# Optimization experiments

Hardware: AMD Instinct MI355X
Metric: run time of the kernel (lower is better)

The kernel has to match this reference:

```python
import jax, jax.numpy as jnp
import numpy as np

B, NG, DEG, CW, OUT = 8, 16384, 16, 64, 256  # graphs, nodes/graph, avg degree, conv_width, output_dim


def _sage(x, src, dst, mask, Wl, bl, Wr):
    # PyG SAGEConv: mean-aggregate neighbors (src -> dst), lin_l(agg)+bias + lin_r(x)
    N = x.shape[0]
    s = jax.ops.segment_sum(x[src] * mask[:, None], dst, num_segments=N)
    c = jax.ops.segment_sum(mask, dst, num_segments=N)
    mean = s / jnp.maximum(c, 1.0)[:, None]
    return mean @ Wl.T + bl + x @ Wr.T


def _gcn(x, src, dst, mask, W, b):
    # PyG GCNConv: self-loops + symmetric deg^{-1/2} normalization; edge_weight == mask
    N = x.shape[0]
    xw = x @ W.T
    deg = 1.0 + jax.ops.segment_sum(mask, dst, num_segments=N)
    dis = jax.lax.rsqrt(deg)
    norm = dis[src] * mask * dis[dst]
    out = jax.ops.segment_sum(xw[src] * norm[:, None], dst, num_segments=N)
    return out + xw * (dis * dis)[:, None] + b


def _topk(x, src, dst, mask, w, n):
    # PyG TopKPooling: score = tanh(x.w/||w||), keep top ceil(0.5*n) per graph,
    # gate kept features by score, re-index edges (here: fixed-size edges + mask)
    score = jnp.tanh((x @ w) / jnp.linalg.norm(w))
    k = (n + 1) // 2
    vals, idx = jax.lax.top_k(score.reshape(B, n), k)  # [B,k], descending like PyG
    perm = (idx + (jnp.arange(B) * n)[:, None]).reshape(-1)  # global old indices
    x_new = x[perm] * vals.reshape(-1)[:, None]
    newpos = jnp.full((B * n,), -1, jnp.int32).at[perm].set(
        jnp.arange(B * k, dtype=jnp.int32))
    ns, nd = newpos[src], newpos[dst]
    m = mask * ((ns >= 0) & (nd >= 0)).astype(x.dtype)
    return x_new, jnp.maximum(ns, 0), jnp.maximum(nd, 0), m, k


def _readout(x, k):
    # [global_max_pool, global_mean_pool] per graph
    xr = x.reshape(B, k, -1)
    return jnp.concatenate([xr.max(axis=1), xr.mean(axis=1)], axis=1)


def setup_inputs() -> dict:
    key = jax.random.key(0)
    ks = jax.random.split(key, 24)
    N, Eg = B * NG, NG * DEG
    off = (jnp.arange(B) * NG)[:, None]
    src = (jax.random.randint(ks[0], (B, Eg), 0, NG) + off).reshape(-1)
    dst = (jax.random.randint(ks[1], (B, Eg), 0, NG) + off).reshape(-1)
    edge_index = jnp.stack([src, dst]).astype(jnp.int32)
    x = jax.random.normal(ks[2], (N, 2), jnp.float32)

    def xav(k, o, i):
        return jax.random.normal(k, (o, i), jnp.float32) * np.float32(np.sqrt(2.0 / (o + i)))

    def vec(k, d):
        return jax.random.normal(k, (d,), jnp.float32) * np.float32(1.0 / np.sqrt(d))

    return dict(
        x=x, edge_index=edge_index,
        Wl1=xav(ks[3], CW, 2), bl1=vec(ks[4], CW), Wr1=xav(ks[5], CW, 2),
        Wl2=xav(ks[6], CW, CW), bl2=vec(ks[7], CW), Wr2=xav(ks[8], CW, CW),
        W4=xav(ks[9], CW, CW), b4=vec(ks[10], CW),
        W5=xav(ks[11], CW, CW), b5=vec(ks[12], CW),
        wp1=vec(ks[13], CW), wp2=vec(ks[14], CW), wp4=vec(ks[15], CW), wp5=vec(ks[16], CW),
        Wa=xav(ks[17], 128, 2 * CW), ba=vec(ks[18], 128),
        Wb=xav(ks[19], 64, 128), bb=vec(ks[20], 64),
        Wc=xav(ks[21], OUT, 64), bc=vec(ks[22], OUT),
    )


def reference(x, edge_index, Wl1, bl1, Wr1, Wl2, bl2, Wr2, W4, b4, W5, b5,
              wp1, wp2, wp4, wp5, Wa, ba, Wb, bb, Wc, bc):
    src, dst = edge_index[0], edge_index[1]
    mask = jnp.ones(src.shape[0], x.dtype)
    n = NG
    h = jax.nn.relu(_sage(x, src, dst, mask, Wl1, bl1, Wr1))
    h, src, dst, mask, n = _topk(h, src, dst, mask, wp1, n)
    x1 = _readout(h, n)
    h = jax.nn.relu(_sage(h, src, dst, mask, Wl2, bl2, Wr2))
    h, src, dst, mask, n = _topk(h, src, dst, mask, wp2, n)
    x2 = _readout(h, n)
    h = jax.nn.relu(_gcn(h, src, dst, mask, W4, b4))
    h, src, dst, mask, n = _topk(h, src, dst, mask, wp4, n)
    x4 = _readout(h, n)
    h = jax.nn.relu(_gcn(h, src, dst, mask, W5, b5))
    h, src, dst, mask, n = _topk(h, src, dst, mask, wp5, n)
    x5 = _readout(h, n)
    z = x1 + x2 + x4 + x5  # [B, 2*CW]
    z = jax.nn.relu(z @ Wa.T + ba)
    z = jax.nn.relu(z @ Wb.T + bb)
    z = z @ Wc.T + bc
    return jax.nn.softmax(z, axis=1)
```

## Files before the change

### kernel.cpp

```cpp
#include <hip/hip_runtime.h>
#include <math.h>

constexpr int Bq  = 8;
constexpr int NGq = 16384;
constexpr int Nq  = Bq * NGq;
constexpr int Eq  = Nq * 16;
constexpr int Eg  = Eq / 8;
constexpr int BCAP = 8192;

constexpr int P1 = 0;
constexpr int P2 = 524288;
constexpr int P3 = 786432;
constexpr int P4 = 917504;
constexpr int PTOT = 983040;

__global__ void k_prep(const float* __restrict__ Wl2, const float* __restrict__ Wr2,
                       const float* __restrict__ W4, const float* __restrict__ W5,
                       const float* __restrict__ Wa, const float* __restrict__ Wb,
                       const float* __restrict__ Wc,
                       const float* __restrict__ w1, const float* __restrict__ w2,
                       const float* __restrict__ w4p, const float* __restrict__ w5p,
                       float* __restrict__ wT, float* __restrict__ wMT,
                       float* __restrict__ winv, int* __restrict__ bcur) {
    int t = threadIdx.x, b = blockIdx.x;
    if (b < 4) {
        const float* in = (b == 0) ? Wl2 : (b == 1) ? Wr2 : (b == 2) ? W4 : W5;
        float* out = wT + (size_t)b * 4096;
        for (int i = t; i < 4096; i += 256) {
            int r = i >> 6, c = i & 63;
            out[c * 64 + r] = in[r * 64 + c];
        }
    } else if (b == 4) {
        float* WaT = wMT;
        for (int i = t; i < 16384; i += 256) {
            int r = i >> 7, c = i & 127;
            WaT[c * 128 + r] = Wa[r * 128 + c];
        }
    } else if (b == 5) {
        float* WbT = wMT + 16384;
        for (int i = t; i < 8192; i += 256) {
            int r = i >> 7, c = i & 127;
            WbT[c * 64 + r] = Wb[r * 128 + c];
        }
    } else if (b == 6) {
        float* WcT = wMT + 16384 + 8192;
        for (int i = t; i < 16384; i += 256) {
            int r = i >> 6, c = i & 63;
            WcT[c * 256 + r] = Wc[r * 64 + c];
        }
    } else {
        int vsel = t >> 6, lane = t & 63;
        const float* wp = (vsel == 0) ? w1 : (vsel == 1) ? w2 : (vsel == 2) ? w4p : w5p;
        float v = wp[lane];
        float ww = v * v;
        for (int o = 32; o; o >>= 1) ww += __shfl_xor(ww, o);
        if (lane == 0) winv[vsel] = 1.0f / sqrtf(ww);
        for (int i = t; i < 512; i += 256) bcur[i] = 0;
    }
}

__global__ void k_csr_a(const int* __restrict__ src, const int* __restrict__ dst,
                        int* __restrict__ bcur, unsigned* __restrict__ pairs) {
    __shared__ int hist[512];
    __shared__ int base[512];
    __shared__ int lcur[512];
    int t = threadIdx.x;
    int blk = blockIdx.x;
    int e0 = blk * 8192;
    int bk[8]; unsigned p[8];
#pragma unroll
    for (int i = 0; i < 8; i++) {
        int e = e0 + i * 1024 + t;
        int d = dst[e];
        bk[i] = d >> 8;
        p[i] = ((unsigned)(d & 255) << 24) | (unsigned)src[e];
    }
    if (t < 512) hist[t] = 0;
    __syncthreads();
#pragma unroll
    for (int i = 0; i < 8; i++) atomicAdd(&hist[bk[i]], 1);
    __syncthreads();
    if (t < 512) {
        int h = hist[t];
        base[t] = h ? atomicAdd(&bcur[t], h) : 0;
        lcur[t] = 0;
    }
    __syncthreads();
#pragma unroll
    for (int i = 0; i < 8; i++) {
        int b = bk[i];
        int r = base[b] + atomicAdd(&lcur[b], 1);
        if (r < BCAP) pairs[(size_t)b * BCAP + r] = p[i];
    }
}

__global__ void k_csr_b(const int* __restrict__ bcnt, const unsigned* __restrict__ pairs,
                        const float2* __restrict__ x2,
                        int* __restrict__ off, int* __restrict__ deg,
                        int* __restrict__ csrc, float2* __restrict__ mean) {
    __shared__ int lcnt[256];
    __shared__ int lcur[256];
    __shared__ int wsum[4];
    int b = blockIdx.x, t = threadIdx.x;
    int beg = b * BCAP;
    int c0 = bcnt[b]; if (c0 > BCAP) c0 = BCAP;
    int end = beg + c0;
    lcnt[t] = 0;
    __syncthreads();
    for (int i = beg + t; i < end; i += 256)
        atomicAdd(&lcnt[pairs[i] >> 24], 1);
    __syncthreads();
    int v = lcnt[t];
    int lane = t & 63, wv = t >> 6;
    int val = v;
    for (int o = 1; o < 64; o <<= 1) {
        int u = __shfl_up(val, o);
        if (lane >= o) val += u;
    }
    if (lane == 63) wsum[wv] = val;
    __syncthreads();
    int add = 0;
    for (int q = 0; q < wv; q++) add += wsum[q];
    int gpos = beg + val + add - v;
    off[b * 256 + t] = gpos;
    deg[b * 256 + t] = v;
    lcur[t] = gpos;
    __syncthreads();
    for (int i = beg + t; i < end; i += 256) {
        unsigned p = pairs[i];
        int pos = atomicAdd(&lcur[p >> 24], 1);
        csrc[pos] = (int)(p & 0x00FFFFFFu);
    }
    __syncthreads();
    float s0 = 0.f, s1 = 0.f;
    for (int e = gpos; e < gpos + v; e++) {
        float2 xv = x2[csrc[e]];
        s0 += xv.x; s1 += xv.y;
    }
    float c = fmaxf((float)v, 1.0f);
    mean[b * 256 + t] = make_float2(s0 / c, s1 / c);
}

__global__ void k_sage1e(const float* __restrict__ x, const float2* __restrict__ mean,
                         const float* __restrict__ Wl, const float* __restrict__ bl,
                         const float* __restrict__ Wr, const float* __restrict__ wp,
                         const float* __restrict__ invn,
                         float* __restrict__ out, float* __restrict__ score) {
    int blk = blockIdx.x;
    int g = blk & 7, i = blk >> 3;
    int wv = threadIdx.x >> 6, j = threadIdx.x & 63;
    int n = g * NGq + i * 4 + wv;
    float2 xn = ((const float2*)x)[n];
    float2 m = mean[n];
    float2 wl = ((const float2*)Wl)[j];
    float2 wr = ((const float2*)Wr)[j];
    float v = wl.x * m.x + wl.y * m.y + bl[j] + wr.x * xn.x + wr.y * xn.y;
    v = fmaxf(v, 0.f);
    out[n * 64 + j] = v;
    float d = v * wp[j];
    for (int o = 32; o; o >>= 1) d += __shfl_xor(d, o);
    if (j == 0) score[n] = d * invn[0];
}

__device__ __forceinline__
void lin_rows(const float* __restrict__ h, const float* __restrict__ WT,
              const float* __restrict__ bias, float* __restrict__ o,
              int Nn, int nblk, int blk0) {
    int j = threadIdx.x & 63, wv = threadIdx.x >> 6;
    float wreg[64];
#pragma unroll
    for (int q = 0; q < 64; q++) wreg[q] = WT[q * 64 + j];
    float bj = bias ? bias[j] : 0.f;
    int stride = nblk * 4;
    for (int n = blk0 * 4 + wv; n < Nn; n += stride) {
        float iv = h[(size_t)n * 64 + j];
        float a0 = 0.f, a1 = 0.f, a2 = 0.f, a3 = 0.f;
#pragma unroll
        for (int q = 0; q < 16; q++) {
            float s0 = __int_as_float(__builtin_amdgcn_readlane(__float_as_int(iv), q));
            float s1 = __int_as_float(__builtin_amdgcn_readlane(__float_as_int(iv), q + 16));
            float s2 = __int_as_float(__builtin_amdgcn_readlane(__float_as_int(iv), q + 32));
            float s3 = __int_as_float(__builtin_amdgcn_readlane(__float_as_int(iv), q + 48));
            a0 += s0 * wreg[q];
            a1 += s1 * wreg[q + 16];
            a2 += s2 * wreg[q + 32];
            a3 += s3 * wreg[q + 48];
        }
        o[(size_t)n * 64 + j] = (a0 + a1) + (a2 + a3) + bj;
    }
}

__global__ __launch_bounds__(256, 4)
void k_linf(const float* __restrict__ h,
            const float* __restrict__ WT1, float* __restrict__ o1, int linB1,
            const float* __restrict__ WT2, const float* __restrict__ bias,
            float* __restrict__ o2, int linB2,
            int Nn,
            const int* __restrict__ off, const int* __restrict__ deg,
            const int* __restrict__ csrc,
            const int* __restrict__ map, const int* __restrict__ orig,
            float* __restrict__ dis, int ng) {
    int blk = blockIdx.x;
    if (blk < linB1) {
        lin_rows(h, WT1, nullptr, o1, Nn, linB1, blk);
    } else if (blk < linB1 + linB2) {
        lin_rows(h, WT2, bias, o2, Nn, linB2, blk - linB1);
    } else {
        int b2 = blk - linB1 - linB2;
        int g = b2 & 7, i = b2 >> 3;
        int wv = threadIdx.x >> 6, j = threadIdx.x & 63;
        int n = g * ng + i * 4 + wv;
        int o = orig[n];
        int beg = off[o], end = beg + deg[o];
        int c = 0;
        for (int base = beg; base < end; base += 64) {
            int d = end - base; if (d > 64) d = 64;
            int cs = (j < d) ? map[csrc[base + j]] : -1;
            c += __popcll(__ballot(cs >= 0));
        }
        if (j == 0) dis[n] = 1.0f / sqrtf(1.0f + (float)c);
    }
}

template<int M>
__global__ void k_topk(float* __restrict__ score, int* __restrict__ newpos,
                       int* __restrict__ perm, int* __restrict__ map, int mode,
                       const int* __restrict__ orig_in, int* __restrict__ orig_out,
                       int og) {
    constexpr int n = M * 1024;
    constexpr int k = n / 2;
    __shared__ unsigned hist[256];
    __shared__ unsigned sh_pfx, sh_msk, sh_rem;
    __shared__ int sh_eqtot, sh_ctr;
    __shared__ int wtot[16];
    __shared__ int runTie, runGt;
    int t = threadIdx.x, b = blockIdx.x;
    int base = b * n;
    int lane = t & 63, wv = t >> 6;

    unsigned kr[M];
#pragma unroll
    for (int i = 0; i < M; i++) {
        unsigned u = __float_as_uint(score[base + t + (i << 10)]);
        kr[i] = u ^ ((u >> 31) ? 0xFFFFFFFFu : 0x80000000u);
    }
    if (t < 256) hist[t] = 0;
    if (t == 0) { sh_pfx = 0; sh_msk = 0; sh_rem = (unsigned)k;
                  sh_eqtot = 0; sh_ctr = 0; runTie = 0; runGt = 0; }
    __syncthreads();

    for (int shift = 24; shift >= 0; shift -= 8) {
        unsigned pfx = sh_pfx, msk = sh_msk;
#pragma unroll
        for (int i = 0; i < M; i++)
            if ((kr[i] & msk) == pfx) atomicAdd(&hist[(kr[i] >> shift) & 255], 1u);
        __syncthreads();
        if (t < 64) {
            unsigned rem = sh_rem;
            unsigned c0 = hist[255 - (t * 4 + 0)];
            unsigned c1 = hist[255 - (t * 4 + 1)];
            unsigned c2 = hist[255 - (t * 4 + 2)];
            unsigned c3 = hist[255 - (t * 4 + 3)];
            unsigned s = c0 + c1 + c2 + c3;
            unsigned sc = s;
            for (int o = 1; o < 64; o <<= 1) {
                unsigned u = __shfl_up(sc, o);
                if (t >= o) sc += u;
            }
            unsigned run = sc - s;
            unsigned cc[4] = {c0, c1, c2, c3};
#pragma unroll
            for (int q = 0; q < 4; q++) {
                unsigned incl = run + cc[q];
                if (run < rem && incl >= rem) {
                    int bb = 255 - (t * 4 + q);
                    sh_rem = rem - run;
                    sh_pfx = pfx | ((unsigned)bb << shift);
                    sh_msk = msk | (255u << shift);
                }
                run = incl;
            }
        }
        __syncthreads();
        if (t < 256) hist[t] = 0;
        __syncthreads();
    }
    unsigned K = sh_pfx;
    int T = (int)sh_rem;

    int le = 0;
#pragma unroll
    for (int i = 0; i < M; i++) le += (kr[i] == K) ? 1 : 0;
    for (int o = 32; o; o >>= 1) le += __shfl_xor(le, o);
    if (lane == 0) atomicAdd(&sh_eqtot, le);
    __syncthreads();

    if (sh_eqtot == T) {
#pragma unroll
        for (int i = 0; i < M; i++) {
            int cur = base + t + (i << 10);
            bool kept = kr[i] >= K;
            unsigned long long mk = __ballot(kept);
            int pos = 0;
            if (mk) {
                int fl = __ffsll(mk) - 1;
                int bp = 0;
                if (lane == fl) bp = atomicAdd(&sh_ctr, __popcll(mk));
                bp = __shfl(bp, fl);
                pos = bp + __popcll(mk & ((1ull << lane) - 1ull));
            }
            if (kept && pos < k) {
                newpos[cur] = b * k + pos;
                perm[b * k + pos] = cur;
                if (og) orig_out[b * k + pos] = (og == 1) ? cur : orig_in[cur];
                unsigned ob = (kr[i] & 0x80000000u) ? (kr[i] ^ 0x80000000u) : ~kr[i];
                score[cur] = tanhf(__uint_as_float(ob));
            } else newpos[cur] = -1;
        }
    } else {
        for (int i = 0; i < M; i++) {
            unsigned key = kr[i];
            int gt = key > K ? 1 : 0;
            int eq = key == K ? 1 : 0;
            int val = (eq << 16) | gt;
            for (int o = 1; o < 64; o <<= 1) {
                int v = __shfl_up(val, o);
                if (lane >= o) val += v;
            }
            if (lane == 63) wtot[wv] = val;
            __syncthreads();
            int add = 0;
            for (int q = 0; q < 16; q++) if (q < wv) add += wtot[q];
            val += add;
            int eqIncl = val >> 16, gtIncl = val & 0xffff;
            int eqExcl = eqIncl - eq, gtExcl = gtIncl - gt;
            int kept = gt | (eq & ((runTie + eqExcl) < T ? 1 : 0));
            int cur = base + t + (i << 10);
            if (kept) {
                int selEqBefore = runTie + eqExcl; if (selEqBefore > T) selEqBefore = T;
                int nl = runGt + gtExcl + selEqBefore;
                if (nl < k) {
                    newpos[cur] = b * k + nl;
                    perm[b * k + nl] = cur;
                    if (og) orig_out[b * k + nl] = (og == 1) ? cur : orig_in[cur];
                    unsigned ob = (key & 0x80000000u) ? (key ^ 0x80000000u) : ~key;
                    score[cur] = tanhf(__uint_as_float(ob));
                } else newpos[cur] = -1;
            } else newpos[cur] = -1;
            __syncthreads();
            if (t == 1023) { runTie += eqIncl; runGt += gtIncl; }
            __syncthreads();
        }
    }

    if (mode) {
        __syncthreads();
        int gbase = b * NGq;
        for (int i2 = t; i2 < NGq; i2 += 1024) {
            int gi = gbase + i2;
            if (mode == 1) map[gi] = newpos[gi];
            else { int m = map[gi]; map[gi] = (m >= 0) ? newpos[m] : -1; }
        }
    }
}

__global__ void k_compact4(const float* __restrict__ hin, const float* __restrict__ score,
                           const int* __restrict__ perm, float* __restrict__ hout, int k,
                           float* __restrict__ partial) {
    __shared__ float sred[2][16][64];
    int blk = blockIdx.x;
    int g = blk & 7, i = blk >> 3;
    int t = threadIdx.x;
    int r = t >> 4, c = t & 15;
    int nn = g * k + i * 16 + r;
    int old = perm[nn];
    float4 v = ((const float4*)(hin + (size_t)old * 64))[c];
    float sc = score[old];
    v.x *= sc; v.y *= sc; v.z *= sc; v.w *= sc;
    ((float4*)(hout + (size_t)nn * 64))[c] = v;
    sred[0][r][c * 4 + 0] = v.x; sred[0][r][c * 4 + 1] = v.y;
    sred[0][r][c * 4 + 2] = v.z; sred[0][r][c * 4 + 3] = v.w;
    sred[1][r][c * 4 + 0] = v.x; sred[1][r][c * 4 + 1] = v.y;
    sred[1][r][c * 4 + 2] = v.z; sred[1][r][c * 4 + 3] = v.w;
    __syncthreads();
    if (t < 64) {
        float mx = sred[0][0][t], sm = sred[1][0][t];
        for (int rr = 1; rr < 16; rr++) {
            mx = fmaxf(mx, sred[0][rr][t]);
            sm += sred[1][rr][t];
        }
        partial[(size_t)blk * 128 + t] = mx;
        partial[(size_t)blk * 128 + 64 + t] = sm;
    }
}

__global__ void k_sage_gather2(const float* __restrict__ gl, const int* __restrict__ off,
                               const int* __restrict__ deg, const int* __restrict__ csrc,
                               const int* __restrict__ map,
                               const int* __restrict__ orig, const float* __restrict__ wp,
                               const float* __restrict__ invn,
                               float* __restrict__ own_in,
                               float* __restrict__ out, float* __restrict__ score, int ng) {
    int blk = blockIdx.x;
    int g = blk & 7, i = blk >> 3;
    int wv = threadIdx.x >> 6, l = threadIdx.x & 63;
    int n = g * ng + i * 4 + wv;
    int o = orig[n];
    int beg = off[o], end = beg + deg[o];
    int fg = l & 15, es = l >> 4;
    float4 own = make_float4(0.f, 0.f, 0.f, 0.f);
    if (es == 0) own = ((const float4*)(own_in + (size_t)n * 64))[fg];
    float4 acc = make_float4(0.f, 0.f, 0.f, 0.f);
    int cnt = 0;
    for (int base = beg; base < end; base += 64) {
        int d = end - base; if (d > 64) d = 64;
        int cs = (l < d) ? map[csrc[base + l]] : -1;
        cnt += __popcll(__ballot(cs >= 0));
        for (int e = 0; e < d; e += 4) {
            int c = __shfl(cs, e + es);
            if (c >= 0) {
                float4 v = ((const float4*)(gl + (size_t)c * 64))[fg];
                acc.x += v.x; acc.y += v.y; acc.z += v.z; acc.w += v.w;
            }
        }
    }
    acc.x += __shfl_xor(acc.x, 16); acc.y += __shfl_xor(acc.y, 16);
    acc.z += __shfl_xor(acc.z, 16); acc.w += __shfl_xor(acc.w, 16);
    acc.x += __shfl_xor(acc.x, 32); acc.y += __shfl_xor(acc.y, 32);
    acc.z += __shfl_xor(acc.z, 32); acc.w += __shfl_xor(acc.w, 32);
    float c = fmaxf((float)cnt, 1.0f);
    float4 v;
    v.x = fmaxf(acc.x / c + own.x, 0.f);
    v.y = fmaxf(acc.y / c + own.y, 0.f);
    v.z = fmaxf(acc.z / c + own.z, 0.f);
    v.w = fmaxf(acc.w / c + own.w, 0.f);
    float dsc = 0.f;
    if (es == 0) {
        ((float4*)(out + (size_t)n * 64))[fg] = v;
        float4 w4 = ((const float4*)wp)[fg];
        dsc = v.x * w4.x + v.y * w4.y + v.z * w4.z + v.w * w4.w;
    }
    for (int o2 = 32; o2; o2 >>= 1) dsc += __shfl_xor(dsc, o2);
    if (l == 0) score[n] = dsc * invn[0];
}

__global__ void k_gcn_gather(const float* __restrict__ xw, const int* __restrict__ off,
                             const int* __restrict__ deg, const int* __restrict__ csrc,
                             const int* __restrict__ map,
                             const int* __restrict__ orig, const float* __restrict__ dis,
                             const float* __restrict__ bb, const float* __restrict__ wp,
                             const float* __restrict__ invn,
                             float* __restrict__ out, float* __restrict__ score, int ng) {
    int blk = blockIdx.x;
    int g = blk & 7, i = blk >> 3;
    int wv = threadIdx.x >> 6, l = threadIdx.x & 63;
    int n = g * ng + i * 4 + wv;
    int o = orig[n];
    int beg = off[o], end = beg + deg[o];
    int fg = l & 15, es = l >> 4;
    float dn = dis[n];
    float4 own = make_float4(0.f, 0.f, 0.f, 0.f);
    if (es == 0) own = ((const float4*)(xw + (size_t)n * 64))[fg];
    float4 acc = make_float4(0.f, 0.f, 0.f, 0.f);
    for (int base = beg; base < end; base += 64) {
        int d = end - base; if (d > 64) d = 64;
        int cs = -1; float dsv = 0.f;
        if (l < d) {
            int cc = map[csrc[base + l]];
            if (cc >= 0) { cs = cc; dsv = dis[cc]; }
        }
        for (int e = 0; e < d; e += 4) {
            int c = __shfl(cs, e + es);
            float dv = __shfl(dsv, e + es);
            if (c >= 0) {
                float4 v = ((const float4*)(xw + (size_t)c * 64))[fg];
                acc.x += v.x * dv; acc.y += v.y * dv;
                acc.z += v.z * dv; acc.w += v.w * dv;
            }
        }
    }
    acc.x += __shfl_xor(acc.x, 16); acc.y += __shfl_xor(acc.y, 16);
    acc.z += __shfl_xor(acc.z, 16); acc.w += __shfl_xor(acc.w, 16);
    acc.x += __shfl_xor(acc.x, 32); acc.y += __shfl_xor(acc.y, 32);
    acc.z += __shfl_xor(acc.z, 32); acc.w += __shfl_xor(acc.w, 32);
    float dsc = 0.f;
    if (es == 0) {
        float4 b4 = ((const float4*)bb)[fg];
        float dd = dn * dn;
        float4 v;
        v.x = fmaxf(acc.x * dn + own.x * dd + b4.x, 0.f);
        v.y = fmaxf(acc.y * dn + own.y * dd + b4.y, 0.f);
        v.z = fmaxf(acc.z * dn + own.z * dd + b4.z, 0.f);
        v.w = fmaxf(acc.w * dn + own.w * dd + b4.w, 0.f);
        ((float4*)(out + (size_t)n * 64))[fg] = v;
        float4 w4 = ((const float4*)wp)[fg];
        dsc = v.x * w4.x + v.y * w4.y + v.z * w4.z + v.w * w4.w;
    }
    for (int o2 = 32; o2; o2 >>= 1) dsc += __shfl_xor(dsc, o2);
    if (l == 0) score[n] = dsc * invn[0];
}

__global__ void k_zred(const float* __restrict__ part, float* __restrict__ red2) {
    __shared__ float sred[2][128];
    int b2 = blockIdx.x;
    int g = b2 & 7, slice = b2 >> 3;
    int t = threadIdx.x;
    int j = t & 127, h = t >> 7;
    int pb0 = slice * 60 + h * 30;
    float accm = -3.0e38f, accs = 0.f;
    for (int pb = pb0; pb < pb0 + 30; pb++) {
        const float* p; int i; float scale;
        if (pb < 512)      { p = part + P1; i = pb;       scale = 1.0f / 8192.0f; }
        else if (pb < 768) { p = part + P2; i = pb - 512; scale = 1.0f / 4096.0f; }
        else if (pb < 896) { p = part + P3; i = pb - 768; scale = 1.0f / 2048.0f; }
        else               { p = part + P4; i = pb - 896; scale = 1.0f / 1024.0f; }
        float v = p[(size_t)(i * 8 + g) * 128 + j];
        accm = fmaxf(accm, v);
        accs += v * scale;
    }
    sred[h][j] = (j < 64) ? accm : accs;
    __syncthreads();
    if (t < 128) {
        float out = (j < 64) ? fmaxf(sred[0][j], sred[1][j]) : (sred[0][j] + sred[1][j]);
        red2[(size_t)b2 * 128 + j] = out;
    }
}

__global__ void k_mlpz(const float* __restrict__ red2,
                       const float* __restrict__ WaT, const float* __restrict__ ba,
                       const float* __restrict__ WbT, const float* __restrict__ bb,
                       const float* __restrict__ WcT, const float* __restrict__ bc,
                       float* __restrict__ out) {
    __shared__ float red[8][128];
    __shared__ float sz[128];
    __shared__ float sa[128];
    __shared__ float sb2[64];
    __shared__ float sc[256];
    __shared__ float tmp[256];
    __shared__ float wred[4];
    int b = blockIdx.x, t = threadIdx.x;
    int j = t & 127, s = t >> 7;
    {
        float v0 = red2[(size_t)((s * 2 + 0) * 8 + b) * 128 + j];
        float v1 = red2[(size_t)((s * 2 + 1) * 8 + b) * 128 + j];
        red[s][j] = (j < 64) ? fmaxf(v0, v1) : (v0 + v1);
    }
    __syncthreads();
    if (t < 128) {
        float zv;
        if (j < 64) {
            float m1 = fmaxf(fmaxf(red[0][j], red[1][j]), fmaxf(red[2][j], red[3][j]));
            float m2 = fmaxf(fmaxf(red[4][j], red[5][j]), fmaxf(red[6][j], red[7][j]));
            zv = fmaxf(m1, m2);
        } else {
            zv = ((red[0][j] + red[1][j]) + (red[2][j] + red[3][j]))
               + ((red[4][j] + red[5][j]) + (red[6][j] + red[7][j]));
        }
        sz[t] = zv;
    }
    __syncthreads();
    if (t < 256) {
        int o = t & 127, half = t >> 7;
        float v = 0.f;
        int q0 = half * 64;
        for (int q = q0; q < q0 + 64; q++) v += sz[q] * WaT[q * 128 + o];
        tmp[t] = v;
    }
    __syncthreads();
    if (t < 128) sa[t] = fmaxf(tmp[t] + tmp[t + 128] + ba[t], 0.f);
    __syncthreads();
    if (t < 256) {
        int o = t & 63, qr = t >> 6;
        float v = 0.f;
        int q0 = qr * 32;
        for (int q = q0; q < q0 + 32; q++) v += sa[q] * WbT[q * 64 + o];
        tmp[t] = v;
    }
    __syncthreads();
    if (t < 64) sb2[t] = fmaxf(tmp[t] + tmp[t + 64] + tmp[t + 128] + tmp[t + 192] + bb[t], 0.f);
    __syncthreads();
    if (t < 256) {
        float v = bc[t];
        for (int q = 0; q < 64; q++) v += sb2[q] * WcT[q * 256 + t];
        sc[t] = v;
    }
    __syncthreads();
    if (t < 256) {
        float m = sc[t];
        for (int o2 = 32; o2; o2 >>= 1) m = fmaxf(m, __shfl_xor(m, o2));
        if ((t & 63) == 0) wred[t >> 6] = m;
    }
    __syncthreads();
    float m = fmaxf(fmaxf(wred[0], wred[1]), fmaxf(wred[2], wred[3]));
    __syncthreads();
    if (t < 256) {
        float e = expf(sc[t] - m);
        tmp[t] = e;
        float ss = e;
        for (int o2 = 32; o2; o2 >>= 1) ss += __shfl_xor(ss, o2);
        if ((t & 63) == 0) wred[t >> 6] = ss;
    }
    __syncthreads();
    if (t < 256) {
        float ss = wred[0] + wred[1] + wred[2] + wred[3];
        out[b * 256 + t] = tmp[t] / ss;
    }
}

extern "C" void kernel_launch(void* const* d_in, const int* in_sizes, int n_in,
                              void* d_out, int out_size, void* d_ws, size_t ws_size,
                              hipStream_t stream) {
    const float* x   = (const float*)d_in[0];
    const int*   ei  = (const int*)d_in[1];
    const int* src = ei;
    const int* dst = ei + Eq;
    const float* Wl1 = (const float*)d_in[2];
    const float* bl1 = (const float*)d_in[3];
    const float* Wr1 = (const float*)d_in[4];
    const float* Wl2 = (const float*)d_in[5];
    const float* bl2 = (const float*)d_in[6];
    const float* Wr2 = (const float*)d_in[7];
    const float* W4  = (const float*)d_in[8];
    const float* b4  = (const float*)d_in[9];
    const float* W5  = (const float*)d_in[10];
    const float* b5  = (const float*)d_in[11];
    const float* wp1 = (const float*)d_in[12];
    const float* wp2 = (const float*)d_in[13];
    const float* wp4 = (const float*)d_in[14];
    const float* wp5 = (const float*)d_in[15];
    const float* Wa  = (const float*)d_in[16];
    const float* ba  = (const float*)d_in[17];
    const float* Wb  = (const float*)d_in[18];
    const float* bbv = (const float*)d_in[19];
    const float* Wc  = (const float*)d_in[20];
    const float* bc  = (const float*)d_in[21];
    float* out = (float*)d_out;

    const int N1 = Nq / 2, N2 = Nq / 4, N3 = Nq / 8, N4 = Nq / 16;

    char* w = (char*)d_ws;
    float* hA    = (float*)w; w += (size_t)Nq * 64 * 4;
    float* hB    = (float*)w; w += (size_t)N1 * 64 * 4;
    float* hC    = (float*)w; w += (size_t)N1 * 64 * 4;
    int*   csrc  = (int*)w;   w += (size_t)512 * BCAP * 4;
    int*   coff  = (int*)w;   w += (size_t)(Nq + 1) * 4;
    int*   degA  = (int*)w;   w += (size_t)Nq * 4;
    int*   bcur  = (int*)w;   w += (size_t)Nq * 4;
    int*   cnt   = (int*)w;   w += (size_t)Nq * 4;
    float* dis   = (float*)w; w += (size_t)Nq * 4;
    float* score = (float*)w; w += (size_t)Nq * 4;
    int*   newpos= (int*)w;   w += (size_t)Nq * 4;
    int*   map   = (int*)w;   w += (size_t)Nq * 4;
    int*   perm  = (int*)w;   w += (size_t)Nq * 4;
    int*   origA = (int*)w;   w += (size_t)Nq * 4;
    int*   origB = (int*)w;   w += (size_t)Nq * 4;
    float* part  = (float*)w; w += (size_t)PTOT * 4;
    float* red2  = (float*)w; w += (size_t)128 * 128 * 4;
    float* wT    = (float*)w; w += 4 * 4096 * 4;
    float* wMT   = (float*)w; w += (16384 + 8192 + 16384) * 4;
    float* WlT2 = wT, *WrT2 = wT + 4096, *W4T = wT + 8192, *W5T = wT + 12288;
    float* WaT = wMT, *WbT = wMT + 16384, *WcT = wMT + 16384 + 8192;
    unsigned* pairs = (unsigned*)hA;
    float2* mean = (float2*)cnt;
    float* winv = (float*)(bcur + 1024);

    k_prep<<<8, 256, 0, stream>>>(Wl2, Wr2, W4, W5, Wa, Wb, Wc,
                                  wp1, wp2, wp4, wp5, wT, wMT, winv, bcur);
    k_csr_a<<<256, 1024, 0, stream>>>(src, dst, bcur, pairs);
    k_csr_b<<<512, 256, 0, stream>>>(bcur, pairs, (const float2*)x, coff, degA, csrc, mean);

    k_sage1e<<<Nq / 4, 256, 0, stream>>>(x, mean, Wl1, bl1, Wr1, wp1, winv, hA, score);
    k_topk<16><<<8, 1024, 0, stream>>>(score, newpos, perm, map, 1, nullptr, origA, 1);
    k_compact4<<<N1 / 16, 256, 0, stream>>>(hA, score, perm, hB, N1 / 8, part + P1);

    k_linf<<<512 + 512, 256, 0, stream>>>(hB,
                                          WlT2, hC, 512,
                                          WrT2, bl2, hA, 512,
                                          N1,
                                          nullptr, nullptr, nullptr, nullptr, nullptr,
                                          nullptr, 0);
    k_sage_gather2<<<N1 / 4, 256, 0, stream>>>(hC, coff, degA, csrc, map, origA,
                                               wp2, winv + 1, hA, hA, score, N1 / 8);
    k_topk<8><<<8, 1024, 0, stream>>>(score, newpos, perm, map, 2, origA, origB, 2);
    k_compact4<<<N2 / 16, 256, 0, stream>>>(hA, score, perm, hB, N2 / 8, part + P2);

    k_linf<<<512 + 8192, 256, 0, stream>>>(hB,
                                           W4T, hC, 512,
                                           nullptr, nullptr, nullptr, 0,
                                           N2,
                                           coff, degA, csrc, map, origB,
                                           dis, N2 / 8);
    k_gcn_gather<<<N2 / 4, 256, 0, stream>>>(hC, coff, degA, csrc, map, origB, dis,
                                             b4, wp4, winv + 2, hA, score, N2 / 8);
    k_topk<4><<<8, 1024, 0, stream>>>(score, newpos, perm, map, 2, origB, origA, 2);
    k_compact4<<<N3 / 16, 256, 0, stream>>>(hA, score, perm, hB, N3 / 8, part + P3);

    k_linf<<<256 + 4096, 256, 0, stream>>>(hB,
                                           W5T, hC, 256,
                                           nullptr, nullptr, nullptr, 0,
                                           N3,
                                           coff, degA, csrc, map, origA,
                                           dis, N3 / 8);
    k_gcn_gather<<<N3 / 4, 256, 0, stream>>>(hC, coff, degA, csrc, map, origA, dis,
                                             b5, wp5, winv + 3, hA, score, N3 / 8);
    k_topk<2><<<8, 1024, 0, stream>>>(score, newpos, perm, map, 0, nullptr, nullptr, 0);
    k_compact4<<<N4 / 16, 256, 0, stream>>>(hA, score, perm, hB, N4 / 8, part + P4);

    k_zred<<<128, 256, 0, stream>>>(part, red2);
    k_mlpz<<<8, 1024, 0, stream>>>(red2, WaT, ba, WbT, bbv, WcT, bc, out);
}
```

Before: 426.1 us.

## Fuse first SAGE layer into CSR build and recompute kept rows in compaction

Removes the separate first-layer SAGE kernel, which wrote the full 131072x64 hidden tensor. The score is now computed per node inside the CSR-building kernel with a 64-iteration scalar loop. The compaction kernel recomputes the 64 features only for the kept nodes from the mean and input. This saves writing and reading a large intermediate, at the cost of redundant arithmetic and a serial per-thread loop in k_csr_b.

```diff
diff --git a/kernel.cpp b/kernel.cpp
--- a/kernel.cpp
+++ b/kernel.cpp
@@ -97,7 +97,10 @@
 __global__ void k_csr_b(const int* __restrict__ bcnt, const unsigned* __restrict__ pairs,
                         const float2* __restrict__ x2,
                         int* __restrict__ off, int* __restrict__ deg,
-                        int* __restrict__ csrc, float2* __restrict__ mean) {
+                        int* __restrict__ csrc, float2* __restrict__ mean,
+                        const float* __restrict__ Wl1, const float* __restrict__ bl1,
+                        const float* __restrict__ Wr1, const float* __restrict__ wp1,
+                        const float* __restrict__ invn, float* __restrict__ score) {
     __shared__ int lcnt[256];
     __shared__ int lcur[256];
     __shared__ int wsum[4];
@@ -138,28 +141,19 @@
         s0 += xv.x; s1 += xv.y;
     }
     float c = fmaxf((float)v, 1.0f);
-    mean[b * 256 + t] = make_float2(s0 / c, s1 / c);
-}
-
-__global__ void k_sage1e(const float* __restrict__ x, const float2* __restrict__ mean,
-                         const float* __restrict__ Wl, const float* __restrict__ bl,
-                         const float* __restrict__ Wr, const float* __restrict__ wp,
-                         const float* __restrict__ invn,
-                         float* __restrict__ out, float* __restrict__ score) {
-    int blk = blockIdx.x;
-    int g = blk & 7, i = blk >> 3;
-    int wv = threadIdx.x >> 6, j = threadIdx.x & 63;
-    int n = g * NGq + i * 4 + wv;
-    float2 xn = ((const float2*)x)[n];
-    float2 m = mean[n];
-    float2 wl = ((const float2*)Wl)[j];
-    float2 wr = ((const float2*)Wr)[j];
-    float v = wl.x * m.x + wl.y * m.y + bl[j] + wr.x * xn.x + wr.y * xn.y;
-    v = fmaxf(v, 0.f);
-    out[n * 64 + j] = v;
-    float d = v * wp[j];
-    for (int o = 32; o; o >>= 1) d += __shfl_xor(d, o);
-    if (j == 0) score[n] = d * invn[0];
+    float m0 = s0 / c, m1 = s1 / c;
+    int n = b * 256 + t;
+    mean[n] = make_float2(m0, m1);
+    float2 xn = x2[n];
+    float dacc = 0.f;
+    for (int jj = 0; jj < 64; jj++) {
+        float2 wl = ((const float2*)Wl1)[jj];
+        float2 wr = ((const float2*)Wr1)[jj];
+        float fv = wl.x * m0 + wl.y * m1 + bl1[jj] + wr.x * xn.x + wr.y * xn.y;
+        fv = fmaxf(fv, 0.f);
+        dacc += fv * wp1[jj];
+    }
+    score[n] = dacc * invn[0];
 }
 
 __device__ __forceinline__
@@ -394,6 +388,50 @@
     }
 }
 
+__global__ void k_compact4r(const float2* __restrict__ mean, const float2* __restrict__ x2,
+                            const float* __restrict__ Wl1, const float* __restrict__ bl1,
+                            const float* __restrict__ Wr1,
+                            const float* __restrict__ score,
+                            const int* __restrict__ perm, float* __restrict__ hout, int k,
+                            float* __restrict__ partial) {
+    __shared__ float sred[2][16][64];
+    int blk = blockIdx.x;
+    int g = blk & 7, i = blk >> 3;
+    int t = threadIdx.x;
+    int r = t >> 4, c = t & 15;
+    int nn = g * k + i * 16 + r;
+    int old = perm[nn];
+    float2 m = mean[old];
+    float2 xn = x2[old];
+    float4 wl01 = ((const float4*)Wl1)[c * 2];
+    float4 wl23 = ((const float4*)Wl1)[c * 2 + 1];
+    float4 wr01 = ((const float4*)Wr1)[c * 2];
+    float4 wr23 = ((const float4*)Wr1)[c * 2 + 1];
+    float4 bl   = ((const float4*)bl1)[c];
+    float4 v;
+    v.x = fmaxf(wl01.x * m.x + wl01.y * m.y + bl.x + wr01.x * xn.x + wr01.y * xn.y, 0.f);
+    v.y = fmaxf(wl01.z * m.x + wl01.w * m.y + bl.y + wr01.z * xn.x + wr01.w * xn.y, 0.f);
+    v.z = fmaxf(wl23.x * m.x + wl23.y * m.y + bl.z + wr23.x * xn.x + wr23.y * xn.y, 0.f);
+    v.w = fmaxf(wl23.z * m.x + wl23.w * m.y + bl.w + wr23.z * xn.x + wr23.w * xn.y, 0.f);
+    float sc = score[old];
+    v.x *= sc; v.y *= sc; v.z *= sc; v.w *= sc;
+    ((float4*)(hout + (size_t)nn * 64))[c] = v;
+    sred[0][r][c * 4 + 0] = v.x; sred[0][r][c * 4 + 1] = v.y;
+    sred[0][r][c * 4 + 2] = v.z; sred[0][r][c * 4 + 3] = v.w;
+    sred[1][r][c * 4 + 0] = v.x; sred[1][r][c * 4 + 1] = v.y;
+    sred[1][r][c * 4 + 2] = v.z; sred[1][r][c * 4 + 3] = v.w;
+    __syncthreads();
+    if (t < 64) {
+        float mx = sred[0][0][t], sm = sred[1][0][t];
+        for (int rr = 1; rr < 16; rr++) {
+            mx = fmaxf(mx, sred[0][rr][t]);
+            sm += sred[1][rr][t];
+        }
+        partial[(size_t)blk * 128 + t] = mx;
+        partial[(size_t)blk * 128 + 64 + t] = sm;
+    }
+}
+
 __global__ void k_sage_gather2(const float* __restrict__ gl, const int* __restrict__ off,
                                const int* __restrict__ deg, const int* __restrict__ csrc,
                                const int* __restrict__ map,
@@ -667,11 +705,12 @@
     k_prep<<<8, 256, 0, stream>>>(Wl2, Wr2, W4, W5, Wa, Wb, Wc,
                                   wp1, wp2, wp4, wp5, wT, wMT, winv, bcur);
     k_csr_a<<<256, 1024, 0, stream>>>(src, dst, bcur, pairs);
-    k_csr_b<<<512, 256, 0, stream>>>(bcur, pairs, (const float2*)x, coff, degA, csrc, mean);
-
-    k_sage1e<<<Nq / 4, 256, 0, stream>>>(x, mean, Wl1, bl1, Wr1, wp1, winv, hA, score);
+    k_csr_b<<<512, 256, 0, stream>>>(bcur, pairs, (const float2*)x, coff, degA, csrc, mean,
+                                     Wl1, bl1, Wr1, wp1, winv, score);
+
     k_topk<16><<<8, 1024, 0, stream>>>(score, newpos, perm, map, 1, nullptr, origA, 1);
-    k_compact4<<<N1 / 16, 256, 0, stream>>>(hA, score, perm, hB, N1 / 8, part + P1);
+    k_compact4r<<<N1 / 16, 256, 0, stream>>>(mean, (const float2*)x, Wl1, bl1, Wr1,
+                                             score, perm, hB, N1 / 8, part + P1);
 
     k_linf<<<512 + 512, 256, 0, stream>>>(hB,
                                           WlT2, hC, 512,
```

Measured after the change: 417.6 us. 1.02x faster.
